# Optimization experiments

Hardware: AMD Instinct MI355X
Metric: run time of the kernel (lower is better)

Reference implementation:

```python
import jax, jax.numpy as jnp
import numpy as np

# per-amino-acid residue lengths (heavy atoms - 1), 20 types, sorted ascending for readability
RES_LEN_NP = np.array([3, 4, 5, 5, 6, 6, 6, 7, 7, 7, 7, 7, 8, 8, 8, 9, 10, 10, 11, 13], dtype=np.int32)
LMAX = int(RES_LEN_NP.max())  # 13
N_TYPES = 20
N_RES = 2048
BATCH = 16
DV_ATM = 64
DV_AMN = 64


def _atoms_for(seq_types_np):
    return int(RES_LEN_NP[seq_types_np].sum())


def setup_inputs() -> dict:
    key = jax.random.key(0)
    k1, k2, k3, k4 = jax.random.split(key, 4)
    seq_np = (np.arange(N_RES) % N_TYPES).astype(np.int32)
    atoms = _atoms_for(seq_np)  # 15036
    pos_atm = jax.random.normal(k1, (BATCH, atoms, 3), dtype=jnp.float32)
    pos_amn = jax.random.normal(k2, (BATCH, N_RES, 3), dtype=jnp.float32)
    scale = 1.0 / np.sqrt(LMAX)
    W_amn = jax.random.normal(k3, (N_TYPES, DV_AMN, LMAX), dtype=jnp.float32) * scale
    W_atm = jax.random.normal(k4, (N_TYPES, LMAX, DV_ATM, LMAX), dtype=jnp.float32) * scale
    return {
        "pos_atm": pos_atm,
        "pos_amn": pos_amn,
        "W_amn": W_amn,
        "W_atm": W_atm,
        "seq_types": jnp.asarray(seq_np),
    }


def reference(pos_atm, pos_amn, W_amn, W_atm, seq_types):
    """Vectorized equivalent of the per-residue loop:
    for each residue i of type t with length L_t:
      diff = pos_atm[:, start_i:start_i+L_t] - pos_amn[:, i, None]        # (B, L_t, 3)
      x_v_amn[:, i] = einsum('ol,bld->bod', W_amn[t, :, :L_t], diff)       # (B, Damn, 3)
      x_v_atm block  = einsum('mvl,bld->bmvd', W_atm[t, :L_t, :, :L_t], diff)
    Residues are padded to LMAX and batched; padding is masked out.
    """
    res_len = jnp.asarray(RES_LEN_NP)
    B, atoms, _ = pos_atm.shape
    lens = res_len[seq_types]                                  # (N,)
    starts = jnp.concatenate([jnp.zeros((1,), lens.dtype), jnp.cumsum(lens)[:-1]])
    ar = jnp.arange(LMAX, dtype=lens.dtype)
    atom_idx = jnp.clip(starts[:, None] + ar[None, :], 0, atoms - 1)  # (N, LMAX)
    mask = ar[None, :] < lens[:, None]                                 # (N, LMAX)

    # diffs: (B, N, LMAX, 3), zeroed at padding
    diffs = (pos_atm[:, atom_idx] - pos_amn[:, :, None, :]) * mask[None, :, :, None]

    Wa = W_amn[seq_types]                                      # (N, Damn, LMAX)
    x_v_amn = jnp.einsum('bnld,nol->bnod', diffs, Wa)          # (B, N, Damn, 3)

    Wt = W_atm[seq_types]                                      # (N, LMAX, Dv, LMAX)
    xa = jnp.einsum('bnld,nmvl->bnmvd', diffs, Wt)             # (B, N, LMAX, Dv, 3)
    xa = xa * mask[None, :, :, None, None]

    # scatter padded per-residue atom outputs back to the flat atom axis;
    # invalid slots go to a dummy row `atoms` that is sliced off
    idx = jnp.where(mask, atom_idx, atoms).reshape(-1)         # (N*LMAX,)
    xa_flat = xa.reshape(B, -1, DV_ATM, 3)                     # (B, N*LMAX, Dv, 3)
    x_v_atm = jnp.zeros((B, atoms + 1, DV_ATM, 3), pos_atm.dtype).at[:, idx].add(xa_flat)[:, :atoms]
    return x_v_atm, x_v_amn
```

## Files before the change

### kernel.cpp

```cpp
#include <hip/hip_runtime.h>

#define N_RES 2048
#define BATCH 16
#define LMAX  13
#define NSLOT 14
#define DV    64
#define DPAD  7

__device__ __constant__ int RES_LEN_D[20] = {3,4,5,5,6,6,6,7,7,7,7,7,8,8,8,9,10,10,11,13};

__global__ __launch_bounds__(256, 3)
void posmix_kernel(const float* __restrict__ pos_atm,
                   const float* __restrict__ pos_amn,
                   const float* __restrict__ W_amn,
                   const float* __restrict__ W_atm,
                   const int*   __restrict__ seq,
                   float* __restrict__ out_atm,
                   float* __restrict__ out_amn,
                   int atoms)
{
  const int i   = blockIdx.x;
  const int tid = threadIdx.x;
  const int t   = seq[i];
  const int L   = RES_LEN_D[t];
  const int Lp1 = L + 1;
  const int Mh  = (Lp1 + 1) >> 1;

  __shared__ float w_lds[NSLOT * LMAX * DV];
  __shared__ float diff_lds[BATCH * LMAX * DPAD];

  int* red = (int*)w_lds;
  {
    int s = 0;
    int base = tid * 8;
    #pragma unroll
    for (int k = 0; k < 8; ++k) {
      int r = base + k;
      if (r < i) s += RES_LEN_D[seq[r]];
    }
    red[tid] = s;
  }
  __syncthreads();
  #pragma unroll
  for (int off = 128; off > 0; off >>= 1) {
    if (tid < off) red[tid] += red[tid + off];
    __syncthreads();
  }
  const int start = red[0];
  __syncthreads();

  if (tid < BATCH * LMAX) {
    int b = tid / LMAX;
    int l = tid - b * LMAX;
    float dx = 0.f, dy = 0.f, dz = 0.f;
    if (l < L) {
      const float* pa = pos_atm + ((size_t)b * atoms + (size_t)(start + l)) * 3;
      const float* pm = pos_amn + ((size_t)b * N_RES + i) * 3;
      dx = pa[0] - pm[0];
      dy = pa[1] - pm[1];
      dz = pa[2] - pm[2];
    }
    float* dd = diff_lds + tid * DPAD;
    dd[0] = dx; dd[1] = dy; dd[2] = dz;
    dd[3] = dx; dd[4] = dy; dd[5] = dz;
  }

  {
    const float* Wt = W_atm + (size_t)t * (LMAX * DV * LMAX);
    const int total = L * DV * LMAX;
    for (int g = tid; g < total; g += 256) {
      int m = g / (DV * LMAX);
      int r = g - m * (DV * LMAX);
      int v = r / LMAX;
      int l = r - v * LMAX;
      w_lds[(m * LMAX + l) * DV + v] = Wt[g];
    }
    const float* Wa = W_amn + (size_t)t * (DV * LMAX);
    for (int g = tid; g < DV * LMAX; g += 256) {
      int o = g / LMAX;
      int l = g - o * LMAX;
      w_lds[(L * LMAX + l) * DV + o] = Wa[g];
    }
  }
  __syncthreads();

  const int ntasks = 48 * 8 * Mh;

  for (int task = tid; task < ntasks; task += 256) {
    int lam = task % 48;
    int rg  = task / 48;
    int mh  = rg % Mh;
    int bh  = rg / Mh;
    int m0  = mh * 2, m1 = m0 + 1;
    int b0  = bh * 2, b1 = b0 + 1;

    int f0 = lam * 4;
    int va = f0 / 3;
    int r  = f0 - va * 3;
    int th = 3 - r;

    const float* w0 = w_lds + (m0 * LMAX) * DV + va;
    const float* w1 = w_lds + (m1 * LMAX) * DV + va;
    const float* p0 = diff_lds + (b0 * LMAX) * DPAD + r;
    const float* p1 = diff_lds + (b1 * LMAX) * DPAD + r;

    float a00[4] = {0.f,0.f,0.f,0.f};
    float a01[4] = {0.f,0.f,0.f,0.f};
    float a10[4] = {0.f,0.f,0.f,0.f};
    float a11[4] = {0.f,0.f,0.f,0.f};

    for (int l = 0; l < L; ++l) {
      float wa0 = w0[l * DV], wb0 = w0[l * DV + 1];
      float wa1 = w1[l * DV], wb1 = w1[l * DV + 1];
      float r0[4], r1[4];
      #pragma unroll
      for (int e = 0; e < 4; ++e) { r0[e] = p0[l * DPAD + e]; r1[e] = p1[l * DPAD + e]; }
      #pragma unroll
      for (int e = 0; e < 4; ++e) {
        float ws0 = (e < th) ? wa0 : wb0;
        float ws1 = (e < th) ? wa1 : wb1;
        a00[e] += ws0 * r0[e];
        a01[e] += ws0 * r1[e];
        a10[e] += ws1 * r0[e];
        a11[e] += ws1 * r1[e];
      }
    }

    {
      float* dst;
      if (m0 < L) dst = out_atm + ((size_t)b0 * atoms + (size_t)(start + m0)) * 192 + f0;
      else        dst = out_amn + ((size_t)b0 * N_RES + i) * 192 + f0;
      *(float4*)dst = make_float4(a00[0], a00[1], a00[2], a00[3]);
      if (m0 < L) dst = out_atm + ((size_t)b1 * atoms + (size_t)(start + m0)) * 192 + f0;
      else        dst = out_amn + ((size_t)b1 * N_RES + i) * 192 + f0;
      *(float4*)dst = make_float4(a01[0], a01[1], a01[2], a01[3]);
    }
    if (m1 <= L) {
      float* dst;
      if (m1 < L) dst = out_atm + ((size_t)b0 * atoms + (size_t)(start + m1)) * 192 + f0;
      else        dst = out_amn + ((size_t)b0 * N_RES + i) * 192 + f0;
      *(float4*)dst = make_float4(a10[0], a10[1], a10[2], a10[3]);
      if (m1 < L) dst = out_atm + ((size_t)b1 * atoms + (size_t)(start + m1)) * 192 + f0;
      else        dst = out_amn + ((size_t)b1 * N_RES + i) * 192 + f0;
      *(float4*)dst = make_float4(a11[0], a11[1], a11[2], a11[3]);
    }
  }
}

extern "C" void kernel_launch(void* const* d_in, const int* in_sizes, int n_in,
                              void* d_out, int out_size, void* d_ws, size_t ws_size,
                              hipStream_t stream) {
  const float* pos_atm = (const float*)d_in[0];
  const float* pos_amn = (const float*)d_in[1];
  const float* W_amn   = (const float*)d_in[2];
  const float* W_atm   = (const float*)d_in[3];
  const int*   seq     = (const int*)d_in[4];

  const int atoms = in_sizes[0] / (BATCH * 3);
  float* out_atm = (float*)d_out;
  float* out_amn = out_atm + (size_t)BATCH * atoms * DV * 3;

  posmix_kernel<<<N_RES, 256, 0, stream>>>(pos_atm, pos_amn, W_amn, W_atm, seq,
                                           out_atm, out_amn, atoms);
}
```

Before: 244.7 us.

## Remap threads to batch×4-channel tiles with register-held diffs and float4 weight reads

Each thread now owns one batch and four output channels and loops over all output rows m, keeping that batch's full diff vector (13×3) in registers. Weight reads from LDS become one float4 per l. The inner loop is fully unrolled to LMAX with zero-padded diffs. The LDS weight row stride is padded to 68 to reduce bank conflicts, and the two weight-loading loops are merged. This removes the per-task index arithmetic, the duplicated diff layout and the select logic, at the cost of wasted FMAs on padded l for short residues, more registers, and three separate float4 stores per thread per row.

```diff
diff --git a/kernel.cpp b/kernel.cpp
--- a/kernel.cpp
+++ b/kernel.cpp
@@ -5,7 +5,7 @@
 #define LMAX  13
 #define NSLOT 14
 #define DV    64
-#define DPAD  7
+#define VSTR  68
 
 __device__ __constant__ int RES_LEN_D[20] = {3,4,5,5,6,6,6,7,7,7,7,7,8,8,8,9,10,10,11,13};
 
@@ -23,13 +23,11 @@
   const int tid = threadIdx.x;
   const int t   = seq[i];
   const int L   = RES_LEN_D[t];
-  const int Lp1 = L + 1;
-  const int Mh  = (Lp1 + 1) >> 1;
 
-  __shared__ float w_lds[NSLOT * LMAX * DV];
-  __shared__ float diff_lds[BATCH * LMAX * DPAD];
+  __shared__ __align__(16) float w_lds[NSLOT * LMAX * VSTR];
+  __shared__ __align__(16) float diff_lds[BATCH * 40];
 
-  int* red = (int*)w_lds;
+  int* red = (int*)diff_lds;
   {
     int s = 0;
     int base = tid * 8;
@@ -49,6 +47,20 @@
   const int start = red[0];
   __syncthreads();
 
+  {
+    const float* Wt = W_atm + (size_t)t * (LMAX * DV * LMAX);
+    const float* Wa = W_amn + (size_t)t * (DV * LMAX);
+    const int total = (L + 1) * (DV * LMAX);
+    for (int g = tid; g < total; g += 256) {
+      int m = g / (DV * LMAX);
+      int r = g - m * (DV * LMAX);
+      int v = r / LMAX;
+      int l = r - v * LMAX;
+      const float* src = (m < L) ? (Wt + (size_t)m * (DV * LMAX)) : Wa;
+      w_lds[(m * LMAX + l) * VSTR + v] = src[r];
+    }
+  }
+
   if (tid < BATCH * LMAX) {
     int b = tid / LMAX;
     int l = tid - b * LMAX;
@@ -60,90 +72,48 @@
       dy = pa[1] - pm[1];
       dz = pa[2] - pm[2];
     }
-    float* dd = diff_lds + tid * DPAD;
+    float* dd = diff_lds + b * 40 + l * 3;
     dd[0] = dx; dd[1] = dy; dd[2] = dz;
-    dd[3] = dx; dd[4] = dy; dd[5] = dz;
+  }
+  if (tid < BATCH) diff_lds[tid * 40 + 39] = 0.f;
+  __syncthreads();
+
+  const int b  = tid >> 4;
+  const int va = tid & 15;
+
+  float df[40] __attribute__((aligned(16)));
+  {
+    const float4* s4 = (const float4*)(diff_lds + b * 40);
+    float4* d4 = (float4*)df;
+    #pragma unroll
+    for (int k = 0; k < 10; ++k) d4[k] = s4[k];
   }
 
-  {
-    const float* Wt = W_atm + (size_t)t * (LMAX * DV * LMAX);
-    const int total = L * DV * LMAX;
-    for (int g = tid; g < total; g += 256) {
-      int m = g / (DV * LMAX);
-      int r = g - m * (DV * LMAX);
-      int v = r / LMAX;
-      int l = r - v * LMAX;
-      w_lds[(m * LMAX + l) * DV + v] = Wt[g];
-    }
-    const float* Wa = W_amn + (size_t)t * (DV * LMAX);
-    for (int g = tid; g < DV * LMAX; g += 256) {
-      int o = g / LMAX;
-      int l = g - o * LMAX;
-      w_lds[(L * LMAX + l) * DV + o] = Wa[g];
-    }
-  }
-  __syncthreads();
+  const float* wbase = w_lds + 4 * va;
 
-  const int ntasks = 48 * 8 * Mh;
+  for (int m = 0; m <= L; ++m) {
+    const float* wr = wbase + (m * LMAX) * VSTR;
 
-  for (int task = tid; task < ntasks; task += 256) {
-    int lam = task % 48;
-    int rg  = task / 48;
-    int mh  = rg % Mh;
-    int bh  = rg / Mh;
-    int m0  = mh * 2, m1 = m0 + 1;
-    int b0  = bh * 2, b1 = b0 + 1;
+    float acc[12];
+    #pragma unroll
+    for (int j = 0; j < 12; ++j) acc[j] = 0.f;
 
-    int f0 = lam * 4;
-    int va = f0 / 3;
-    int r  = f0 - va * 3;
-    int th = 3 - r;
-
-    const float* w0 = w_lds + (m0 * LMAX) * DV + va;
-    const float* w1 = w_lds + (m1 * LMAX) * DV + va;
-    const float* p0 = diff_lds + (b0 * LMAX) * DPAD + r;
-    const float* p1 = diff_lds + (b1 * LMAX) * DPAD + r;
-
-    float a00[4] = {0.f,0.f,0.f,0.f};
-    float a01[4] = {0.f,0.f,0.f,0.f};
-    float a10[4] = {0.f,0.f,0.f,0.f};
-    float a11[4] = {0.f,0.f,0.f,0.f};
-
-    for (int l = 0; l < L; ++l) {
-      float wa0 = w0[l * DV], wb0 = w0[l * DV + 1];
-      float wa1 = w1[l * DV], wb1 = w1[l * DV + 1];
-      float r0[4], r1[4];
-      #pragma unroll
-      for (int e = 0; e < 4; ++e) { r0[e] = p0[l * DPAD + e]; r1[e] = p1[l * DPAD + e]; }
-      #pragma unroll
-      for (int e = 0; e < 4; ++e) {
-        float ws0 = (e < th) ? wa0 : wb0;
-        float ws1 = (e < th) ? wa1 : wb1;
-        a00[e] += ws0 * r0[e];
-        a01[e] += ws0 * r1[e];
-        a10[e] += ws1 * r0[e];
-        a11[e] += ws1 * r1[e];
-      }
+    #pragma unroll
+    for (int l = 0; l < LMAX; ++l) {
+      float4 w = *(const float4*)(wr + l * VSTR);
+      float dx = df[3*l + 0], dy = df[3*l + 1], dz = df[3*l + 2];
+      acc[0]  += w.x * dx; acc[1]  += w.x * dy; acc[2]  += w.x * dz;
+      acc[3]  += w.y * dx; acc[4]  += w.y * dy; acc[5]  += w.y * dz;
+      acc[6]  += w.z * dx; acc[7]  += w.z * dy; acc[8]  += w.z * dz;
+      acc[9]  += w.w * dx; acc[10] += w.w * dy; acc[11] += w.w * dz;
     }
 
-    {
-      float* dst;
-      if (m0 < L) dst = out_atm + ((size_t)b0 * atoms + (size_t)(start + m0)) * 192 + f0;
-      else        dst = out_amn + ((size_t)b0 * N_RES + i) * 192 + f0;
-      *(float4*)dst = make_float4(a00[0], a00[1], a00[2], a00[3]);
-      if (m0 < L) dst = out_atm + ((size_t)b1 * atoms + (size_t)(start + m0)) * 192 + f0;
-      else        dst = out_amn + ((size_t)b1 * N_RES + i) * 192 + f0;
-      *(float4*)dst = make_float4(a01[0], a01[1], a01[2], a01[3]);
-    }
-    if (m1 <= L) {
-      float* dst;
-      if (m1 < L) dst = out_atm + ((size_t)b0 * atoms + (size_t)(start + m1)) * 192 + f0;
-      else        dst = out_amn + ((size_t)b0 * N_RES + i) * 192 + f0;
-      *(float4*)dst = make_float4(a10[0], a10[1], a10[2], a10[3]);
-      if (m1 < L) dst = out_atm + ((size_t)b1 * atoms + (size_t)(start + m1)) * 192 + f0;
-      else        dst = out_amn + ((size_t)b1 * N_RES + i) * 192 + f0;
-      *(float4*)dst = make_float4(a11[0], a11[1], a11[2], a11[3]);
-    }
+    float* dst = (m < L)
+      ? out_atm + ((size_t)b * atoms + (size_t)(start + m)) * 192 + va * 12
+      : out_amn + ((size_t)b * N_RES + i) * 192 + va * 12;
+    *(float4*)(dst + 0) = make_float4(acc[0], acc[1],  acc[2],  acc[3]);
+    *(float4*)(dst + 4) = make_float4(acc[4], acc[5],  acc[6],  acc[7]);
+    *(float4*)(dst + 8) = make_float4(acc[8], acc[9],  acc[10], acc[11]);
   }
 }
 
```

Result: no change. 245.3 us (+0.3%).
